# Optimization experiments

Measured on AMD Instinct MI355X. Metric: run time of the kernel, lower is better.

The kernel has to match this reference:

```python
import jax, jax.numpy as jnp
import numpy as np

B, L, H, E = 4, 2048, 8, 64  # S == L

def setup_inputs() -> dict:
    key = jax.random.key(0)
    k1, k2, k3, k4, k5 = jax.random.split(key, 5)
    q = jax.random.normal(k1, (B, L, H, E), dtype=jnp.float32)
    k = jax.random.normal(k2, (B, L, H, E), dtype=jnp.float32)
    v = jax.random.normal(k3, (B, L, H, E), dtype=jnp.float32)
    tau = jax.random.uniform(k4, (B, 1), dtype=jnp.float32) + 0.5  # positive scale
    delta = jax.random.normal(k5, (B, L), dtype=jnp.float32) * 0.1
    return {"q": q, "k": k, "v": v, "tau": tau, "delta": delta}

def reference(q, k, v, tau, delta):
    # De-stationarized attention: scores = (QK^T) * tau + delta, softmax(scale*scores)
    E_ = q.shape[-1]
    scale = 1.0 / jnp.sqrt(jnp.float32(E_))
    # tau: [B,1] -> [B,1,1,1]; delta: [B,S] -> [B,1,1,S]
    scores = jnp.einsum('blhe,bshe->bhls', q, k) * tau[:, None, None] + delta[:, None, None, :]
    a = jax.nn.softmax(scale * scores, axis=-1)  # dropout is identity in eval / p=0
    out = jnp.einsum('bhls,bshd->blhd', a, v)
    return out, a
```

## Files before the change

kernel.cpp:

```cpp
#include <hip/hip_runtime.h>
#include <stdint.h>

#define B_ 4
#define L_ 2048
#define H_ 8
#define E_ 64
#define S_ 2048
#define QT 16
#define SROW 2056

typedef __bf16 bf16x8 __attribute__((ext_vector_type(8)));
typedef _Float16 f16x8 __attribute__((ext_vector_type(8)));
typedef float f32x4 __attribute__((ext_vector_type(4)));
typedef unsigned short u16;
typedef u16 u16x4 __attribute__((ext_vector_type(4)));
typedef u16 u16x8 __attribute__((ext_vector_type(8)));

__device__ __forceinline__ u16 f32_to_bf16(float f) {
  union { float f; uint32_t u; } x;
  x.f = f;
  uint32_t u = x.u;
  return (u16)((u + 0x7FFFu + ((u >> 16) & 1u)) >> 16);
}

__global__ __launch_bounds__(256) void prep_qkd(
    const float* __restrict__ q, const float* __restrict__ k,
    const float* __restrict__ tau, const float* __restrict__ delta,
    u16* __restrict__ qb, u16* __restrict__ kb, float* __restrict__ dl) {
  int idx = blockIdx.x * 256 + threadIdx.x;
  int i4 = idx * 4;
  int b = i4 >> 20;
  float ts = tau[b] * 0.125f;
  f32x4 qv = *(const f32x4*)(q + i4);
  f32x4 kv = *(const f32x4*)(k + i4);
  u16x4 qs, ks;
#pragma unroll
  for (int j = 0; j < 4; ++j) {
    qs[j] = f32_to_bf16(qv[j] * ts);
    ks[j] = f32_to_bf16(kv[j]);
  }
  *(u16x4*)(qb + i4) = qs;
  *(u16x4*)(kb + i4) = ks;
  if (idx < (B_ * S_) / 4) {
    f32x4 dv = *(const f32x4*)(delta + i4);
    f32x4 ds = {dv[0] * 0.125f, dv[1] * 0.125f, dv[2] * 0.125f, dv[3] * 0.125f};
    *(f32x4*)(dl + i4) = ds;
  }
}

__global__ __launch_bounds__(256) void prep_v(const float* __restrict__ v,
                                              u16* __restrict__ vb) {
  __shared__ float t[32][33];
  int bid = blockIdx.x;
  int et = bid & 1;
  int st = (bid >> 1) & 63;
  int h = (bid >> 7) & 7;
  int b = bid >> 10;
  int tx = threadIdx.x & 31;
  int ty = threadIdx.x >> 5;
#pragma unroll
  for (int k2 = 0; k2 < 4; ++k2) {
    int s = st * 32 + ty + 8 * k2;
    int e = et * 32 + tx;
    t[ty + 8 * k2][tx] = v[(((size_t)b * S_ + s) * H_ + h) * E_ + e];
  }
  __syncthreads();
#pragma unroll
  for (int k2 = 0; k2 < 4; ++k2) {
    int e = et * 32 + ty + 8 * k2;
    int s = st * 32 + tx;
    vb[(((size_t)b * H_ + h) * E_ + e) * S_ + s] = f32_to_bf16(t[tx][ty + 8 * k2]);
  }
}

__global__ __launch_bounds__(256, 2) void attn_main(
    const u16* __restrict__ qb, const u16* __restrict__ kb,
    const u16* __restrict__ vb, const float* __restrict__ dl,
    float* __restrict__ out, float* __restrict__ oa) {
  __shared__ _Float16 sc[QT][SROW];
  __shared__ float zinv[QT];

  int bid = blockIdx.x;
  int swz = (bid & 7) * 512 + (bid >> 3);
  int b = swz >> 10;
  int h = (swz >> 7) & 7;
  int qt = swz & 127;
  int m0 = qt * QT;

  int tid = threadIdx.x;
  int lane = tid & 63;
  int wave = tid >> 6;
  int l15 = lane & 15;
  int l4 = lane >> 4;

  bf16x8 qa0, qa1;
  {
    const u16* qp = qb + (((size_t)b * L_ + (m0 + l15)) * H_ + h) * E_ + 8 * l4;
    qa0 = *(const bf16x8*)(qp);
    qa1 = *(const bf16x8*)(qp + 32);
  }

  {
    const u16* kbase =
        kb + (((size_t)b * S_ + (wave * 512 + l15)) * H_ + h) * E_ + 8 * l4;
    const float* dbase = dl + b * S_ + wave * 512 + l15;
    int r0 = l4 * 4;
    int colbase = wave * 512 + l15;
#pragma unroll 2
    for (int c = 0; c < 32; ++c) {
      const u16* kp = kbase + (size_t)c * 16 * H_ * E_;
      f32x4 acc = {0.f, 0.f, 0.f, 0.f};
      acc = __builtin_amdgcn_mfma_f32_16x16x32_bf16(qa0, *(const bf16x8*)(kp), acc, 0, 0, 0);
      acc = __builtin_amdgcn_mfma_f32_16x16x32_bf16(qa1, *(const bf16x8*)(kp + 32), acc, 0, 0, 0);
      float d = dbase[c * 16];
      int col = colbase + c * 16;
      sc[r0 + 0][col] = (_Float16)(acc[0] + d);
      sc[r0 + 1][col] = (_Float16)(acc[1] + d);
      sc[r0 + 2][col] = (_Float16)(acc[2] + d);
      sc[r0 + 3][col] = (_Float16)(acc[3] + d);
    }
  }
  __syncthreads();

  {
    const float LOG2E = 1.44269504088896f;
#pragma unroll 1
    for (int rr = 0; rr < 4; ++rr) {
      int row = wave * 4 + rr;
      f16x8 hv[4];
#pragma unroll
      for (int c2 = 0; c2 < 4; ++c2)
        hv[c2] = *(const f16x8*)&sc[row][c2 * 512 + lane * 8];
      float mx = -3.0e38f;
#pragma unroll
      for (int c2 = 0; c2 < 4; ++c2)
#pragma unroll
        for (int j = 0; j < 8; ++j) mx = fmaxf(mx, (float)hv[c2][j]);
      for (int o = 32; o > 0; o >>= 1) mx = fmaxf(mx, __shfl_xor(mx, o, 64));
      float p[32];
      float sum = 0.f;
#pragma unroll
      for (int c2 = 0; c2 < 4; ++c2)
#pragma unroll
        for (int j = 0; j < 8; ++j) {
          float e = __builtin_amdgcn_exp2f(((float)hv[c2][j] - mx) * LOG2E);
          p[c2 * 8 + j] = e;
          sum += e;
        }
      for (int o = 32; o > 0; o >>= 1) sum += __shfl_xor(sum, o, 64);
      float zi = 1.f / sum;
      if (lane == 0) zinv[row] = zi;
      float* arow = oa + ((size_t)(b * H_ + h) * L_ + (m0 + row)) * S_;
#pragma unroll
      for (int c2 = 0; c2 < 4; ++c2) {
        int sbase = c2 * 512 + lane * 8;
        f32x4 w0 = {p[c2 * 8 + 0] * zi, p[c2 * 8 + 1] * zi, p[c2 * 8 + 2] * zi,
                    p[c2 * 8 + 3] * zi};
        f32x4 w1 = {p[c2 * 8 + 4] * zi, p[c2 * 8 + 5] * zi, p[c2 * 8 + 6] * zi,
                    p[c2 * 8 + 7] * zi};
        *(f32x4*)(arow + sbase) = w0;
        *(f32x4*)(arow + sbase + 4) = w1;
        u16x8 pk;
#pragma unroll
        for (int j = 0; j < 8; ++j) pk[j] = f32_to_bf16(p[c2 * 8 + j]);
        *(u16x8*)((u16*)&sc[row][sbase]) = pk;
      }
    }
  }
  __syncthreads();

  {
    int e0 = wave * 16;
    const u16* vbase =
        vb + ((size_t)(b * H_ + h) * E_ + e0 + l15) * S_ + 8 * l4;
    const u16* scb = (const u16*)&sc[l15][0] + 8 * l4;
    f32x4 oacc = {0.f, 0.f, 0.f, 0.f};
#pragma unroll 4
    for (int c = 0; c < 64; ++c) {
      bf16x8 pa = *(const bf16x8*)(scb + c * 32);
      bf16x8 vf = *(const bf16x8*)(vbase + c * 32);
      oacc = __builtin_amdgcn_mfma_f32_16x16x32_bf16(pa, vf, oacc, 0, 0, 0);
    }
    int r0 = l4 * 4;
#pragma unroll
    for (int r = 0; r < 4; ++r) {
      int row = r0 + r;
      out[(((size_t)b * L_ + (m0 + row)) * H_ + h) * E_ + e0 + l15] =
          oacc[r] * zinv[row];
    }
  }
}

extern "C" void kernel_launch(void* const* d_in, const int* in_sizes, int n_in,
                              void* d_out, int out_size, void* d_ws, size_t ws_size,
                              hipStream_t stream) {
  (void)in_sizes; (void)n_in; (void)out_size;
  const float* q = (const float*)d_in[0];
  const float* k = (const float*)d_in[1];
  const float* v = (const float*)d_in[2];
  const float* tau = (const float*)d_in[3];
  const float* delta = (const float*)d_in[4];
  float* out = (float*)d_out;
  float* oa = out + (size_t)B_ * L_ * H_ * E_;

  const size_t NQ = (size_t)B_ * L_ * H_ * E_;
  u16* qb = (u16*)d_ws;
  u16* kb = qb + NQ;
  u16* vb = kb + NQ;
  float* dl = (float*)(vb + NQ);
  size_t need = 3 * NQ * sizeof(u16) + (size_t)B_ * S_ * sizeof(float);
  if (ws_size < need) return;

  prep_qkd<<<4096, 256, 0, stream>>>(q, k, tau, delta, qb, kb, dl);
  prep_v<<<4096, 256, 0, stream>>>(v, vb);
  attn_main<<<4096, 256, 0, stream>>>(qb, kb, vb, dl, out, oa);
}
```

Before: 326.2 us.

## Replace LDS score buffer with per-wave two-pass recompute of QK^T scores

Each wave now owns a whole 16-row query tile instead of four waves sharing one tile through a large LDS score buffer. A first pass computes QK^T and accumulates exp sums without max subtraction. A second pass recomputes the scores, writes the normalized attention matrix, and feeds bf16 probabilities through a small per-wave LDS tile into the PV MFMA. This removes the 64KB shared buffer to raise occupancy, at the cost of computing QK^T twice. Dropping the max subtraction risks overflow for large scores.

```diff
diff --git a/kernel.cpp b/kernel.cpp
--- a/kernel.cpp
+++ b/kernel.cpp
@@ -7,20 +7,23 @@
 #define E_ 64
 #define S_ 2048
 #define QT 16
-#define SROW 2056
 
 typedef __bf16 bf16x8 __attribute__((ext_vector_type(8)));
-typedef _Float16 f16x8 __attribute__((ext_vector_type(8)));
 typedef float f32x4 __attribute__((ext_vector_type(4)));
 typedef unsigned short u16;
 typedef u16 u16x4 __attribute__((ext_vector_type(4)));
-typedef u16 u16x8 __attribute__((ext_vector_type(8)));
 
 __device__ __forceinline__ u16 f32_to_bf16(float f) {
   union { float f; uint32_t u; } x;
   x.f = f;
   uint32_t u = x.u;
   return (u16)((u + 0x7FFFu + ((u >> 16) & 1u)) >> 16);
+}
+
+__device__ __forceinline__ float bf16_to_f32(u16 h) {
+  union { uint32_t u; float f; } x;
+  x.u = ((uint32_t)h) << 16;
+  return x.f;
 }
 
 __global__ __launch_bounds__(256) void prep_qkd(
@@ -73,25 +76,27 @@
   }
 }
 
-__global__ __launch_bounds__(256, 2) void attn_main(
+__global__ __launch_bounds__(256, 4) void attn_fused(
     const u16* __restrict__ qb, const u16* __restrict__ kb,
     const u16* __restrict__ vb, const float* __restrict__ dl,
     float* __restrict__ out, float* __restrict__ oa) {
-  __shared__ _Float16 sc[QT][SROW];
-  __shared__ float zinv[QT];
+  __shared__ __align__(16) u16 pt[4][16][40];
+  __shared__ float zsh[4][16];
 
   int bid = blockIdx.x;
-  int swz = (bid & 7) * 512 + (bid >> 3);
-  int b = swz >> 10;
-  int h = (swz >> 7) & 7;
-  int qt = swz & 127;
-  int m0 = qt * QT;
-
+  int swz = (bid & 7) * 128 + (bid >> 3);
   int tid = threadIdx.x;
   int lane = tid & 63;
   int wave = tid >> 6;
+  int t = swz * 4 + wave;
+  int b = t >> 10;
+  int h = (t >> 7) & 7;
+  int qt = t & 127;
+  int m0 = qt * QT;
   int l15 = lane & 15;
   int l4 = lane >> 4;
+
+  const float LOG2E = 1.44269504088896f;
 
   bf16x8 qa0, qa1;
   {
@@ -100,93 +105,90 @@
     qa1 = *(const bf16x8*)(qp + 32);
   }
 
-  {
-    const u16* kbase =
-        kb + (((size_t)b * S_ + (wave * 512 + l15)) * H_ + h) * E_ + 8 * l4;
-    const float* dbase = dl + b * S_ + wave * 512 + l15;
-    int r0 = l4 * 4;
-    int colbase = wave * 512 + l15;
-#pragma unroll 2
-    for (int c = 0; c < 32; ++c) {
-      const u16* kp = kbase + (size_t)c * 16 * H_ * E_;
+  const u16* kbase = kb + (((size_t)b * S_ + l15) * H_ + h) * E_ + 8 * l4;
+  const float* dbase = dl + b * S_ + l15;
+
+  float sums[4] = {0.f, 0.f, 0.f, 0.f};
+#pragma unroll 4
+  for (int c = 0; c < 128; ++c) {
+    const u16* kp = kbase + (size_t)c * (16 * H_ * E_);
+    f32x4 acc = {0.f, 0.f, 0.f, 0.f};
+    acc = __builtin_amdgcn_mfma_f32_16x16x32_bf16(qa0, *(const bf16x8*)(kp), acc, 0, 0, 0);
+    acc = __builtin_amdgcn_mfma_f32_16x16x32_bf16(qa1, *(const bf16x8*)(kp + 32), acc, 0, 0, 0);
+    float d = dbase[c * 16];
+#pragma unroll
+    for (int r = 0; r < 4; ++r)
+      sums[r] += __builtin_amdgcn_exp2f((acc[r] + d) * LOG2E);
+  }
+#pragma unroll
+  for (int r = 0; r < 4; ++r) {
+    sums[r] += __shfl_xor(sums[r], 1, 64);
+    sums[r] += __shfl_xor(sums[r], 2, 64);
+    sums[r] += __shfl_xor(sums[r], 4, 64);
+    sums[r] += __shfl_xor(sums[r], 8, 64);
+  }
+  float zinv[4];
+#pragma unroll
+  for (int r = 0; r < 4; ++r) zinv[r] = 1.f / sums[r];
+  if (l15 == 0) {
+#pragma unroll
+    for (int r = 0; r < 4; ++r) zsh[wave][4 * l4 + r] = zinv[r];
+  }
+  __syncthreads();
+  float zrow = zsh[wave][l15];
+
+  f32x4 oacc[4];
+#pragma unroll
+  for (int et = 0; et < 4; ++et) oacc[et] = (f32x4){0.f, 0.f, 0.f, 0.f};
+
+  float* arow = oa + (((size_t)(b * H_ + h)) * L_ + (m0 + l15)) * S_ + 8 * l4;
+  const u16* vb0 = vb + ((size_t)(b * H_ + h) * E_ + l15) * S_ + 8 * l4;
+  u16* ptw = &pt[wave][0][0];
+
+#pragma unroll 1
+  for (int c2 = 0; c2 < 64; ++c2) {
+#pragma unroll
+    for (int cc = 0; cc < 2; ++cc) {
+      int c = 2 * c2 + cc;
+      const u16* kp = kbase + (size_t)c * (16 * H_ * E_);
       f32x4 acc = {0.f, 0.f, 0.f, 0.f};
       acc = __builtin_amdgcn_mfma_f32_16x16x32_bf16(qa0, *(const bf16x8*)(kp), acc, 0, 0, 0);
       acc = __builtin_amdgcn_mfma_f32_16x16x32_bf16(qa1, *(const bf16x8*)(kp + 32), acc, 0, 0, 0);
       float d = dbase[c * 16];
-      int col = colbase + c * 16;
-      sc[r0 + 0][col] = (_Float16)(acc[0] + d);
-      sc[r0 + 1][col] = (_Float16)(acc[1] + d);
-      sc[r0 + 2][col] = (_Float16)(acc[2] + d);
-      sc[r0 + 3][col] = (_Float16)(acc[3] + d);
-    }
-  }
-  __syncthreads();
-
-  {
-    const float LOG2E = 1.44269504088896f;
-#pragma unroll 1
-    for (int rr = 0; rr < 4; ++rr) {
-      int row = wave * 4 + rr;
-      f16x8 hv[4];
-#pragma unroll
-      for (int c2 = 0; c2 < 4; ++c2)
-        hv[c2] = *(const f16x8*)&sc[row][c2 * 512 + lane * 8];
-      float mx = -3.0e38f;
-#pragma unroll
-      for (int c2 = 0; c2 < 4; ++c2)
-#pragma unroll
-        for (int j = 0; j < 8; ++j) mx = fmaxf(mx, (float)hv[c2][j]);
-      for (int o = 32; o > 0; o >>= 1) mx = fmaxf(mx, __shfl_xor(mx, o, 64));
-      float p[32];
-      float sum = 0.f;
-#pragma unroll
-      for (int c2 = 0; c2 < 4; ++c2)
-#pragma unroll
-        for (int j = 0; j < 8; ++j) {
-          float e = __builtin_amdgcn_exp2f(((float)hv[c2][j] - mx) * LOG2E);
-          p[c2 * 8 + j] = e;
-          sum += e;
-        }
-      for (int o = 32; o > 0; o >>= 1) sum += __shfl_xor(sum, o, 64);
-      float zi = 1.f / sum;
-      if (lane == 0) zinv[row] = zi;
-      float* arow = oa + ((size_t)(b * H_ + h) * L_ + (m0 + row)) * S_;
-#pragma unroll
-      for (int c2 = 0; c2 < 4; ++c2) {
-        int sbase = c2 * 512 + lane * 8;
-        f32x4 w0 = {p[c2 * 8 + 0] * zi, p[c2 * 8 + 1] * zi, p[c2 * 8 + 2] * zi,
-                    p[c2 * 8 + 3] * zi};
-        f32x4 w1 = {p[c2 * 8 + 4] * zi, p[c2 * 8 + 5] * zi, p[c2 * 8 + 6] * zi,
-                    p[c2 * 8 + 7] * zi};
-        *(f32x4*)(arow + sbase) = w0;
-        *(f32x4*)(arow + sbase + 4) = w1;
-        u16x8 pk;
-#pragma unroll
-        for (int j = 0; j < 8; ++j) pk[j] = f32_to_bf16(p[c2 * 8 + j]);
-        *(u16x8*)((u16*)&sc[row][sbase]) = pk;
+#pragma unroll
+      for (int r = 0; r < 4; ++r) {
+        float p = __builtin_amdgcn_exp2f((acc[r] + d) * LOG2E);
+        ptw[(4 * l4 + r) * 40 + cc * 16 + l15] = f32_to_bf16(p);
       }
     }
-  }
-  __syncthreads();
-
-  {
-    int e0 = wave * 16;
-    const u16* vbase =
-        vb + ((size_t)(b * H_ + h) * E_ + e0 + l15) * S_ + 8 * l4;
-    const u16* scb = (const u16*)&sc[l15][0] + 8 * l4;
-    f32x4 oacc = {0.f, 0.f, 0.f, 0.f};
-#pragma unroll 4
-    for (int c = 0; c < 64; ++c) {
-      bf16x8 pa = *(const bf16x8*)(scb + c * 32);
-      bf16x8 vf = *(const bf16x8*)(vbase + c * 32);
-      oacc = __builtin_amdgcn_mfma_f32_16x16x32_bf16(pa, vf, oacc, 0, 0, 0);
-    }
-    int r0 = l4 * 4;
+    asm volatile("" ::: "memory");
+    bf16x8 pa = *(const bf16x8*)(ptw + l15 * 40 + 8 * l4);
+    asm volatile("" ::: "memory");
+
+    union { u16x4 h4; uint64_t u; } lo_u, hi_u;
+    f32x4 alo, ahi;
+#pragma unroll
+    for (int j = 0; j < 4; ++j) {
+      alo[j] = (float)pa[j] * zrow;
+      ahi[j] = (float)pa[j + 4] * zrow;
+    }
+    *(f32x4*)(arow + (size_t)c2 * 32) = alo;
+    *(f32x4*)(arow + (size_t)c2 * 32 + 4) = ahi;
+
+#pragma unroll
+    for (int et = 0; et < 4; ++et) {
+      bf16x8 vf = *(const bf16x8*)(vb0 + (size_t)et * 16 * S_ + c2 * 32);
+      oacc[et] = __builtin_amdgcn_mfma_f32_16x16x32_bf16(pa, vf, oacc[et], 0, 0, 0);
+    }
+  }
+
+#pragma unroll
+  for (int et = 0; et < 4; ++et) {
 #pragma unroll
     for (int r = 0; r < 4; ++r) {
-      int row = r0 + r;
-      out[(((size_t)b * L_ + (m0 + row)) * H_ + h) * E_ + e0 + l15] =
-          oacc[r] * zinv[row];
+      int row = 4 * l4 + r;
+      out[(((size_t)b * L_ + (m0 + row)) * H_ + h) * E_ + et * 16 + l15] =
+          oacc[et][r] * zinv[r];
     }
   }
 }
@@ -213,5 +215,5 @@
 
   prep_qkd<<<4096, 256, 0, stream>>>(q, k, tau, delta, qb, kb, dl);
   prep_v<<<4096, 256, 0, stream>>>(v, vb);
-  attn_main<<<4096, 256, 0, stream>>>(qb, kb, vb, dl, out, oa);
-}
+  attn_fused<<<1024, 256, 0, stream>>>(qb, kb, vb, dl, out, oa);
+}
```

New measurement: 434.8 us. 1.33x slower.
